# Kernel tuning notes

Measured on AMD Instinct MI355X. Metric: run time of the kernel, lower is better.

The kernel has to match this reference:

```python
import jax, jax.numpy as jnp
import numpy as np

N, C, H, W = 16, 256, 128, 128
TC = max(8, C // 32)  # temp_c
EPS = 1e-5


def setup_inputs() -> dict:
    key = jax.random.key(0)
    ks = jax.random.split(key, 10)
    x = jax.random.normal(ks[0], (N, C, H, W), jnp.float32)
    # conv1: 1x1, C -> TC (weight squeezed to [TC, C])
    w1 = jax.random.normal(ks[1], (TC, C), jnp.float32) * 0.05
    b1 = jnp.zeros((TC,), jnp.float32)
    # BatchNorm2d (inference form)
    bn_gamma = jnp.ones((TC,), jnp.float32)
    bn_beta = jnp.zeros((TC,), jnp.float32)
    bn_mean = jnp.zeros((TC,), jnp.float32)
    bn_var = jnp.ones((TC,), jnp.float32)
    # conv2: kernel (1,2), TC -> C, squeezed to [C, TC, 2]
    w2 = jax.random.normal(ks[2], (C, TC, 2), jnp.float32) * 0.1
    b2 = jnp.zeros((C,), jnp.float32)
    # conv3: kernel (2,1), TC -> C, squeezed to [C, TC, 2]
    w3 = jax.random.normal(ks[3], (C, TC, 2), jnp.float32) * 0.1
    b3 = jnp.zeros((C,), jnp.float32)
    # conv4: kernel (1,2), TC -> C, squeezed to [C, TC, 2]
    w4 = jax.random.normal(ks[4], (C, TC, 2), jnp.float32) * 0.1
    b4 = jnp.zeros((C,), jnp.float32)
    return dict(x=x, w1=w1, b1=b1, bn_gamma=bn_gamma, bn_beta=bn_beta,
                bn_mean=bn_mean, bn_var=bn_var, w2=w2, b2=b2, w3=w3, b3=b3,
                w4=w4, b4=b4)


def reference(x, w1, b1, bn_gamma, bn_beta, bn_mean, bn_var,
              w2, b2, w3, b3, w4, b4):
    n, c, Hh, Ww = x.shape
    # avg/max pools along W (per-row), H (per-col), and global (per-channel)
    cat_h = jnp.stack([x.mean(3), x.max(3)], axis=-1)            # [n,c,H,2]
    cat_w = jnp.stack([x.mean(2), x.max(2)], axis=-1)            # [n,c,W,2]
    cat_c = jnp.stack([x.mean((2, 3)), x.max((2, 3))], -1)[:, :, None, :]  # [n,c,1,2]
    x_cat = jnp.concatenate([cat_h, cat_w, cat_c], axis=2)       # [n,c,H+W+1,2]
    # 1x1 conv + BN (inference) + h_swish
    y = jnp.einsum('ncsk,tc->ntsk', x_cat, w1) + b1[None, :, None, None]
    inv = bn_gamma / jnp.sqrt(bn_var + EPS)
    y = (y - bn_mean[None, :, None, None]) * inv[None, :, None, None] \
        + bn_beta[None, :, None, None]
    y = y * jnp.clip(y + 3.0, 0.0, 6.0) / 6.0                    # h_swish
    # split
    xh = y[:, :, :Hh, :]               # [n,tc,H,2]
    xw = y[:, :, Hh:Hh + Ww, :]        # [n,tc,W,2]
    xc = y[:, :, Hh + Ww, :]           # [n,tc,2]
    # tiny convs (kernels collapse to contractions over (tc, k)) + sigmoid
    a_h = jax.nn.sigmoid(jnp.einsum('nthk,otk->noh', xh, w2) + b2[None, :, None])  # [n,C,H]
    a_w = jax.nn.sigmoid(jnp.einsum('ntwk,otk->now', xw, w3) + b3[None, :, None])  # [n,C,W]
    a_c = jax.nn.sigmoid(jnp.einsum('ntk,otk->no', xc, w4) + b4[None, :])          # [n,C]
    return x * a_w[:, :, None, :] * a_h[:, :, :, None] * a_c[:, :, None, None]
```

## Files before the change

### kernel.cpp

```cpp
#include <hip/hip_runtime.h>
#include <math.h>

#define N_ 16
#define C_ 256
#define H_ 128
#define W_ 128
#define TC_ 8
#define S_ 257
#define EPS_ 1e-5f
#define NBLK 512
#define BPN 32

#define XCT_OFF  0
#define AH_OFF   2105344
#define AW_OFF   (AH_OFF + 524288)
#define Y256_OFF (AW_OFF + 524288)

typedef float f4n __attribute__((ext_vector_type(4)));

template <int CTRL>
__device__ __forceinline__ float dpp_zf(float x) {
    return __int_as_float(__builtin_amdgcn_update_dpp(
        0, __float_as_int(x), CTRL, 0xF, 0xF, true));
}
template <int CTRL>
__device__ __forceinline__ float dpp_keep(float x) {
    return __int_as_float(__builtin_amdgcn_update_dpp(
        __float_as_int(x), __float_as_int(x), CTRL, 0xF, 0xF, false));
}
#define SHR1 0x111
#define SHR2 0x112
#define SHR4 0x114
#define SHR8 0x118
#define BC15 0x142

__device__ __forceinline__ float rowsum32(float x) {
    x += dpp_zf<SHR1>(x);
    x += dpp_zf<SHR2>(x);
    x += dpp_zf<SHR4>(x);
    x += dpp_zf<SHR8>(x);
    x += dpp_zf<BC15>(x);
    return x;
}
__device__ __forceinline__ float rowmax32(float x) {
    x = fmaxf(x, dpp_keep<SHR1>(x));
    x = fmaxf(x, dpp_keep<SHR2>(x));
    x = fmaxf(x, dpp_keep<SHR4>(x));
    x = fmaxf(x, dpp_keep<SHR8>(x));
    x = fmaxf(x, dpp_keep<BC15>(x));
    return x;
}

__global__ __launch_bounds__(256, 4) void k1_stats(
    const float* __restrict__ x, float* __restrict__ xcat)
{
    const int tid = threadIdx.x, lane = tid & 63, wv = tid >> 6;
    const int p = blockIdx.x * 4 + wv;
    const float4* xt = reinterpret_cast<const float4*>(x) + (size_t)p * 4096;
    float2* xcat2 = reinterpret_cast<float2*>(xcat) + (size_t)p * S_;

    float4 cs = make_float4(0.f, 0.f, 0.f, 0.f);
    float4 cm = make_float4(-INFINITY, -INFINITY, -INFINITY, -INFINITY);

    #pragma unroll 8
    for (int it = 0; it < 64; ++it) {
        const float4 v = xt[it * 64 + lane];
        cs.x += v.x; cs.y += v.y; cs.z += v.z; cs.w += v.w;
        cm.x = fmaxf(cm.x, v.x); cm.y = fmaxf(cm.y, v.y);
        cm.z = fmaxf(cm.z, v.z); cm.w = fmaxf(cm.w, v.w);

        float rs = (v.x + v.y) + (v.z + v.w);
        float rm = fmaxf(fmaxf(v.x, v.y), fmaxf(v.z, v.w));
        rs = rowsum32(rs);
        rm = rowmax32(rm);
        if ((lane & 31) == 31)
            xcat2[it * 2 + (lane >> 5)] = make_float2(rs * (1.f / 128.f), rm);
    }

    cs.x += __shfl_xor(cs.x, 32); cs.y += __shfl_xor(cs.y, 32);
    cs.z += __shfl_xor(cs.z, 32); cs.w += __shfl_xor(cs.w, 32);
    cm.x = fmaxf(cm.x, __shfl_xor(cm.x, 32));
    cm.y = fmaxf(cm.y, __shfl_xor(cm.y, 32));
    cm.z = fmaxf(cm.z, __shfl_xor(cm.z, 32));
    cm.w = fmaxf(cm.w, __shfl_xor(cm.w, 32));

    if (lane < 32) {
        const int w0 = 4 * lane;
        xcat2[128 + w0 + 0] = make_float2(cs.x * (1.f / 128.f), cm.x);
        xcat2[128 + w0 + 1] = make_float2(cs.y * (1.f / 128.f), cm.y);
        xcat2[128 + w0 + 2] = make_float2(cs.z * (1.f / 128.f), cm.z);
        xcat2[128 + w0 + 3] = make_float2(cs.w * (1.f / 128.f), cm.w);
    }

    float gs = (cs.x + cs.y) + (cs.z + cs.w);
    float gm = fmaxf(fmaxf(cm.x, cm.y), fmaxf(cm.z, cm.w));
    #pragma unroll
    for (int m = 16; m >= 1; m >>= 1) {
        gs += __shfl_xor(gs, m);
        gm = fmaxf(gm, __shfl_xor(gm, m));
    }
    if (lane == 0) xcat2[256] = make_float2(gs * (1.f / 16384.f), gm);
}

__global__ __launch_bounds__(256, 2) void k2_attn(
    const float* __restrict__ xcat,
    const float* __restrict__ w1, const float* __restrict__ b1,
    const float* __restrict__ gam, const float* __restrict__ bet,
    const float* __restrict__ mu, const float* __restrict__ var,
    const float* __restrict__ w2, const float* __restrict__ b2,
    const float* __restrict__ w3, const float* __restrict__ b3,
    float* __restrict__ ahg, float* __restrict__ awg, float* __restrict__ y256g)
{
    const int b = blockIdx.x;
    const int n = b >> 5, cg = b & 31;
    const int tid = threadIdx.x;
    __shared__ __align__(16) float smf[6448];

    float* w1s = smf;
    float* red = smf + 2048;
    float* ys  = smf + 6272;
    const float2* xc2 = reinterpret_cast<const float2*>(xcat) + (size_t)n * C_ * S_;
    const int s0 = cg * 8;

    for (int i = tid; i < TC_ * C_; i += 256) w1s[i] = w1[i];
    __syncthreads();

    {
        const int cgrp = tid >> 3, si = tid & 7;
        const int s = s0 + si;
        float acc[16];
        #pragma unroll
        for (int j = 0; j < 16; ++j) acc[j] = 0.f;
        #pragma unroll
        for (int i = 0; i < 8; ++i) {
            const int c = cgrp * 8 + i;
            const float2 v = xc2[c * S_ + s];
            #pragma unroll
            for (int t = 0; t < TC_; ++t) {
                const float w = w1s[t * C_ + c];
                acc[t * 2 + 0] += v.x * w;
                acc[t * 2 + 1] += v.y * w;
            }
        }
        #pragma unroll
        for (int j = 0; j < 16; ++j) red[(si * 16 + j) * 33 + cgrp] = acc[j];
    }
    __syncthreads();

    if (tid < 128) {
        const int si2 = tid >> 4, j = tid & 15, t = j >> 1;
        float z = 0.f;
        #pragma unroll
        for (int g = 0; g < 32; ++g) z += red[(si2 * 16 + j) * 33 + g];
        const float inv = gam[t] * rsqrtf(var[t] + EPS_);
        float y = (z + b1[t] - mu[t]) * inv + bet[t];
        y = y * fminf(fmaxf(y + 3.f, 0.f), 6.f) * (1.f / 6.f);
        ys[si2 * 17 + j] = y;
    }
    __syncthreads();

    if (cg == BPN - 1) {
        const int c = tid;
        const float2 v = xc2[c * S_ + 256];
        float pj[16];
        #pragma unroll
        for (int t = 0; t < TC_; ++t) {
            const float w = w1s[t * C_ + c];
            pj[t * 2 + 0] = v.x * w;
            pj[t * 2 + 1] = v.y * w;
        }
        __syncthreads();
        float* red2 = smf;
        float* redB = smf + 4400;
        #pragma unroll
        for (int j = 0; j < 16; ++j) red2[tid * 17 + j] = pj[j];
        __syncthreads();
        {
            const int g = tid >> 4, j = tid & 15;
            float z = 0.f;
            #pragma unroll
            for (int m = 0; m < 16; ++m) z += red2[(g * 16 + m) * 17 + j];
            redB[j * 17 + g] = z;
        }
        __syncthreads();
        if (tid < 16) {
            const int j = tid, t = j >> 1;
            float z = 0.f;
            #pragma unroll
            for (int g = 0; g < 16; ++g) z += redB[j * 17 + g];
            const float inv = gam[t] * rsqrtf(var[t] + EPS_);
            float y = (z + b1[t] - mu[t]) * inv + bet[t];
            y = y * fminf(fmaxf(y + 3.f, 0.f), 6.f) * (1.f / 6.f);
            y256g[n * 16 + j] = y;
        }
        __syncthreads();
    }

    {
        const int o = tid;
        const bool is_h = (cg < 16);
        const float* wX = is_h ? w2 : w3;
        const float zb = is_h ? b2[o] : b3[o];
        float4 wr[4];
        const float4* wv = reinterpret_cast<const float4*>(wX + o * 16);
        #pragma unroll
        for (int q = 0; q < 4; ++q) wr[q] = wv[q];

        float r[8];
        #pragma unroll
        for (int si = 0; si < 8; ++si) {
            float z = zb;
            #pragma unroll
            for (int q = 0; q < 4; ++q) {
                z += ys[si * 17 + q * 4 + 0] * wr[q].x
                   + ys[si * 17 + q * 4 + 1] * wr[q].y
                   + ys[si * 17 + q * 4 + 2] * wr[q].z
                   + ys[si * 17 + q * 4 + 3] * wr[q].w;
            }
            r[si] = 1.f / (1.f + expf(-z));
        }
        float* og = is_h ? (ahg + (size_t)(n * C_ + o) * H_ + s0)
                         : (awg + (size_t)(n * C_ + o) * W_ + (s0 - 128));
        *reinterpret_cast<float4*>(og)     = make_float4(r[0], r[1], r[2], r[3]);
        *reinterpret_cast<float4*>(og + 4) = make_float4(r[4], r[5], r[6], r[7]);
    }
}

__global__ __launch_bounds__(256, 4) void k3_apply(
    const float* __restrict__ x,
    const float* __restrict__ w4, const float* __restrict__ b4,
    const float* __restrict__ ahg, const float* __restrict__ awg,
    const float* __restrict__ y256g, float* __restrict__ out)
{
    const int tid = threadIdx.x, lane = tid & 63, wv = tid >> 6;
    const int p = blockIdx.x * 4 + wv;
    const int n = p >> 8, o = p & 255;

    float z = b4[o];
    const float4* w4v = reinterpret_cast<const float4*>(w4 + o * 16);
    const float4* yv  = reinterpret_cast<const float4*>(y256g + n * 16);
    #pragma unroll
    for (int q = 0; q < 4; ++q) {
        const float4 ww = w4v[q], yy = yv[q];
        z += yy.x * ww.x + yy.y * ww.y + yy.z * ww.z + yy.w * ww.w;
    }
    const float ac = 1.f / (1.f + expf(-z));

    const float4 aw = reinterpret_cast<const float4*>(awg + (size_t)p * W_)[lane & 31];

    const f4n* x4 = reinterpret_cast<const f4n*>(x) + (size_t)p * 4096;
    f4n* o4 = reinterpret_cast<f4n*>(out) + (size_t)p * 4096;
    const float* ah = ahg + (size_t)p * H_;
    const int half = lane >> 5;

    #pragma unroll 8
    for (int it = 0; it < 64; ++it) {
        f4n v = x4[it * 64 + lane];
        const float s = ac * ah[2 * it + half];
        v.x *= s * aw.x; v.y *= s * aw.y; v.z *= s * aw.z; v.w *= s * aw.w;
        __builtin_nontemporal_store(v, &o4[it * 64 + lane]);
    }
}

extern "C" void kernel_launch(void* const* d_in, const int* in_sizes, int n_in,
                              void* d_out, int out_size, void* d_ws, size_t ws_size,
                              hipStream_t stream) {
    const float* x   = (const float*)d_in[0];
    const float* w1  = (const float*)d_in[1];
    const float* b1  = (const float*)d_in[2];
    const float* gam = (const float*)d_in[3];
    const float* bet = (const float*)d_in[4];
    const float* mu  = (const float*)d_in[5];
    const float* var = (const float*)d_in[6];
    const float* w2  = (const float*)d_in[7];
    const float* b2  = (const float*)d_in[8];
    const float* w3  = (const float*)d_in[9];
    const float* b3  = (const float*)d_in[10];
    const float* w4  = (const float*)d_in[11];
    const float* b4  = (const float*)d_in[12];

    float* ws    = (float*)d_ws;
    float* xcat  = ws + XCT_OFF;
    float* ahg   = ws + AH_OFF;
    float* awg   = ws + AW_OFF;
    float* y256g = ws + Y256_OFF;
    float* out   = (float*)d_out;

    k1_stats<<<1024, 256, 0, stream>>>(x, xcat);
    k2_attn<<<NBLK, 256, 0, stream>>>(xcat, w1, b1, gam, bet, mu, var,
                                      w2, b2, w3, b3, ahg, awg, y256g);
    k3_apply<<<1024, 256, 0, stream>>>(x, w4, b4, ahg, awg, y256g, out);
}
```

Before: 155.2 us.

## Fuse three kernels into one persistent kernel with per-batch atomic barriers

The three launches (stats, attention, apply) become one kernel with one block per (n,c) plane. Each block holds its 64KB plane in registers, so x is read from HBM only once instead of twice. Per-batch global atomic counters act as barriers between the stats, attention and apply phases, and a memset resets them each call. The kernel needs all 4096 blocks to be co-resident or it can deadlock, and the register-held tile plus spin waits may reduce occupancy.

```diff
diff --git a/kernel.cpp b/kernel.cpp
--- a/kernel.cpp
+++ b/kernel.cpp
@@ -8,13 +8,13 @@
 #define TC_ 8
 #define S_ 257
 #define EPS_ 1e-5f
-#define NBLK 512
-#define BPN 32
+#define NBLK 4096
 
 #define XCT_OFF  0
 #define AH_OFF   2105344
 #define AW_OFF   (AH_OFF + 524288)
 #define Y256_OFF (AW_OFF + 524288)
+#define CNT_OFF  (Y256_OFF + 256)
 
 typedef float f4n __attribute__((ext_vector_type(4)));
 
@@ -51,20 +51,34 @@
     return x;
 }
 
-__global__ __launch_bounds__(256, 4) void k1_stats(
-    const float* __restrict__ x, float* __restrict__ xcat)
+__global__ __launch_bounds__(256, 4) void mega(
+    const float* __restrict__ x,
+    const float* __restrict__ w1, const float* __restrict__ b1,
+    const float* __restrict__ gam, const float* __restrict__ bet,
+    const float* __restrict__ mu, const float* __restrict__ var,
+    const float* __restrict__ w2, const float* __restrict__ b2,
+    const float* __restrict__ w3, const float* __restrict__ b3,
+    const float* __restrict__ w4, const float* __restrict__ b4,
+    float* __restrict__ xcat, float* __restrict__ ahg, float* __restrict__ awg,
+    float* __restrict__ y256g, unsigned* __restrict__ cnt,
+    float* __restrict__ out)
 {
+    const int b = blockIdx.x;
+    const int n = b >> 8, c = b & 255;
     const int tid = threadIdx.x, lane = tid & 63, wv = tid >> 6;
-    const int p = blockIdx.x * 4 + wv;
-    const float4* xt = reinterpret_cast<const float4*>(x) + (size_t)p * 4096;
-    float2* xcat2 = reinterpret_cast<float2*>(xcat) + (size_t)p * S_;
-
+    __shared__ __align__(16) float smf[6448];
+
+    const f4n* x4 = reinterpret_cast<const f4n*>(x) + (size_t)b * 4096;
+    float2* xcat2 = reinterpret_cast<float2*>(xcat) + (size_t)b * S_;
+
+    f4n xr[16];
     float4 cs = make_float4(0.f, 0.f, 0.f, 0.f);
     float4 cm = make_float4(-INFINITY, -INFINITY, -INFINITY, -INFINITY);
 
-    #pragma unroll 8
-    for (int it = 0; it < 64; ++it) {
-        const float4 v = xt[it * 64 + lane];
+    #pragma unroll
+    for (int it = 0; it < 16; ++it) {
+        xr[it] = x4[it * 256 + tid];
+        const f4n v = xr[it];
         cs.x += v.x; cs.y += v.y; cs.z += v.z; cs.w += v.w;
         cm.x = fmaxf(cm.x, v.x); cm.y = fmaxf(cm.y, v.y);
         cm.z = fmaxf(cm.z, v.z); cm.w = fmaxf(cm.w, v.w);
@@ -74,7 +88,8 @@
         rs = rowsum32(rs);
         rm = rowmax32(rm);
         if ((lane & 31) == 31)
-            xcat2[it * 2 + (lane >> 5)] = make_float2(rs * (1.f / 128.f), rm);
+            xcat2[it * 8 + wv * 2 + (lane >> 5)] =
+                make_float2(rs * (1.f / 128.f), rm);
     }
 
     cs.x += __shfl_xor(cs.x, 32); cs.y += __shfl_xor(cs.y, 32);
@@ -84,181 +99,203 @@
     cm.z = fmaxf(cm.z, __shfl_xor(cm.z, 32));
     cm.w = fmaxf(cm.w, __shfl_xor(cm.w, 32));
 
-    if (lane < 32) {
-        const int w0 = 4 * lane;
-        xcat2[128 + w0 + 0] = make_float2(cs.x * (1.f / 128.f), cm.x);
-        xcat2[128 + w0 + 1] = make_float2(cs.y * (1.f / 128.f), cm.y);
-        xcat2[128 + w0 + 2] = make_float2(cs.z * (1.f / 128.f), cm.z);
-        xcat2[128 + w0 + 3] = make_float2(cs.w * (1.f / 128.f), cm.w);
-    }
-
-    float gs = (cs.x + cs.y) + (cs.z + cs.w);
-    float gm = fmaxf(fmaxf(cm.x, cm.y), fmaxf(cm.z, cm.w));
-    #pragma unroll
-    for (int m = 16; m >= 1; m >>= 1) {
-        gs += __shfl_xor(gs, m);
-        gm = fmaxf(gm, __shfl_xor(gm, m));
-    }
-    if (lane == 0) xcat2[256] = make_float2(gs * (1.f / 16384.f), gm);
-}
-
-__global__ __launch_bounds__(256, 2) void k2_attn(
-    const float* __restrict__ xcat,
-    const float* __restrict__ w1, const float* __restrict__ b1,
-    const float* __restrict__ gam, const float* __restrict__ bet,
-    const float* __restrict__ mu, const float* __restrict__ var,
-    const float* __restrict__ w2, const float* __restrict__ b2,
-    const float* __restrict__ w3, const float* __restrict__ b3,
-    float* __restrict__ ahg, float* __restrict__ awg, float* __restrict__ y256g)
-{
-    const int b = blockIdx.x;
-    const int n = b >> 5, cg = b & 31;
-    const int tid = threadIdx.x;
-    __shared__ __align__(16) float smf[6448];
-
-    float* w1s = smf;
-    float* red = smf + 2048;
-    float* ys  = smf + 6272;
-    const float2* xc2 = reinterpret_cast<const float2*>(xcat) + (size_t)n * C_ * S_;
-    const int s0 = cg * 8;
-
-    for (int i = tid; i < TC_ * C_; i += 256) w1s[i] = w1[i];
+    {
+        float4* scr_s = reinterpret_cast<float4*>(smf);
+        float4* scr_m = reinterpret_cast<float4*>(smf) + 128;
+        if (lane < 32) {
+            scr_s[wv * 32 + lane] = make_float4(cs.x, cs.y, cs.z, cs.w);
+            scr_m[wv * 32 + lane] = make_float4(cm.x, cm.y, cm.z, cm.w);
+        }
+        __syncthreads();
+
+        if (tid < 32) {
+            const float4 s0 = scr_s[tid],      s1 = scr_s[32 + tid],
+                         s2 = scr_s[64 + tid], s3 = scr_s[96 + tid];
+            const float4 m0 = scr_m[tid],      m1 = scr_m[32 + tid],
+                         m2 = scr_m[64 + tid], m3 = scr_m[96 + tid];
+            float4 S, M;
+            S.x = (s0.x + s1.x) + (s2.x + s3.x);
+            S.y = (s0.y + s1.y) + (s2.y + s3.y);
+            S.z = (s0.z + s1.z) + (s2.z + s3.z);
+            S.w = (s0.w + s1.w) + (s2.w + s3.w);
+            M.x = fmaxf(fmaxf(m0.x, m1.x), fmaxf(m2.x, m3.x));
+            M.y = fmaxf(fmaxf(m0.y, m1.y), fmaxf(m2.y, m3.y));
+            M.z = fmaxf(fmaxf(m0.z, m1.z), fmaxf(m2.z, m3.z));
+            M.w = fmaxf(fmaxf(m0.w, m1.w), fmaxf(m2.w, m3.w));
+
+            const int w0 = 4 * tid;
+            xcat2[128 + w0 + 0] = make_float2(S.x * (1.f / 128.f), M.x);
+            xcat2[128 + w0 + 1] = make_float2(S.y * (1.f / 128.f), M.y);
+            xcat2[128 + w0 + 2] = make_float2(S.z * (1.f / 128.f), M.z);
+            xcat2[128 + w0 + 3] = make_float2(S.w * (1.f / 128.f), M.w);
+
+            float gs = (S.x + S.y) + (S.z + S.w);
+            float gm = fmaxf(fmaxf(M.x, M.y), fmaxf(M.z, M.w));
+            #pragma unroll
+            for (int m = 16; m >= 1; m >>= 1) {
+                gs += __shfl_xor(gs, m);
+                gm = fmaxf(gm, __shfl_xor(gm, m));
+            }
+            if (tid == 0) xcat2[256] = make_float2(gs * (1.f / 16384.f), gm);
+        }
+        __syncthreads();
+    }
+
+    if (tid == 0) {
+        unsigned* c1 = cnt + n * 64;
+        __hip_atomic_fetch_add(c1, 1u, __ATOMIC_RELEASE, __HIP_MEMORY_SCOPE_AGENT);
+        while (__hip_atomic_load(c1, __ATOMIC_RELAXED, __HIP_MEMORY_SCOPE_AGENT) < 256u)
+            __builtin_amdgcn_s_sleep(16);
+        (void)__hip_atomic_load(c1, __ATOMIC_ACQUIRE, __HIP_MEMORY_SCOPE_AGENT);
+    }
     __syncthreads();
 
-    {
-        const int cgrp = tid >> 3, si = tid & 7;
-        const int s = s0 + si;
-        float acc[16];
-        #pragma unroll
-        for (int j = 0; j < 16; ++j) acc[j] = 0.f;
-        #pragma unroll
-        for (int i = 0; i < 8; ++i) {
-            const int c = cgrp * 8 + i;
-            const float2 v = xc2[c * S_ + s];
-            #pragma unroll
-            for (int t = 0; t < TC_; ++t) {
-                const float w = w1s[t * C_ + c];
-                acc[t * 2 + 0] += v.x * w;
-                acc[t * 2 + 1] += v.y * w;
-            }
-        }
-        #pragma unroll
-        for (int j = 0; j < 16; ++j) red[(si * 16 + j) * 33 + cgrp] = acc[j];
-    }
-    __syncthreads();
-
-    if (tid < 128) {
-        const int si2 = tid >> 4, j = tid & 15, t = j >> 1;
-        float z = 0.f;
-        #pragma unroll
-        for (int g = 0; g < 32; ++g) z += red[(si2 * 16 + j) * 33 + g];
-        const float inv = gam[t] * rsqrtf(var[t] + EPS_);
-        float y = (z + b1[t] - mu[t]) * inv + bet[t];
-        y = y * fminf(fmaxf(y + 3.f, 0.f), 6.f) * (1.f / 6.f);
-        ys[si2 * 17 + j] = y;
-    }
-    __syncthreads();
-
-    if (cg == BPN - 1) {
-        const int c = tid;
-        const float2 v = xc2[c * S_ + 256];
-        float pj[16];
-        #pragma unroll
-        for (int t = 0; t < TC_; ++t) {
-            const float w = w1s[t * C_ + c];
-            pj[t * 2 + 0] = v.x * w;
-            pj[t * 2 + 1] = v.y * w;
-        }
-        __syncthreads();
-        float* red2 = smf;
-        float* redB = smf + 4400;
-        #pragma unroll
-        for (int j = 0; j < 16; ++j) red2[tid * 17 + j] = pj[j];
-        __syncthreads();
+    if (c < 32) {
+        float* w1s = smf;
+        float* red = smf + 2048;
+        float* ys  = smf + 6272;
+        const float2* xc2 = reinterpret_cast<const float2*>(xcat) + (size_t)n * C_ * S_;
+        const int s0 = c * 8;
+
+        for (int i = tid; i < TC_ * C_; i += 256) w1s[i] = w1[i];
+        __syncthreads();
+
         {
-            const int g = tid >> 4, j = tid & 15;
+            const int cgrp = tid >> 3, si = tid & 7;
+            const int s = s0 + si;
+            float acc[16];
+            #pragma unroll
+            for (int j = 0; j < 16; ++j) acc[j] = 0.f;
+            #pragma unroll
+            for (int i = 0; i < 8; ++i) {
+                const int cc = cgrp * 8 + i;
+                const float2 v = xc2[cc * S_ + s];
+                #pragma unroll
+                for (int t = 0; t < TC_; ++t) {
+                    const float w = w1s[t * C_ + cc];
+                    acc[t * 2 + 0] += v.x * w;
+                    acc[t * 2 + 1] += v.y * w;
+                }
+            }
+            #pragma unroll
+            for (int j = 0; j < 16; ++j) red[(si * 16 + j) * 33 + cgrp] = acc[j];
+        }
+        __syncthreads();
+
+        if (tid < 128) {
+            const int si2 = tid >> 4, j = tid & 15, t = j >> 1;
             float z = 0.f;
             #pragma unroll
-            for (int m = 0; m < 16; ++m) z += red2[(g * 16 + m) * 17 + j];
-            redB[j * 17 + g] = z;
-        }
-        __syncthreads();
-        if (tid < 16) {
-            const int j = tid, t = j >> 1;
-            float z = 0.f;
-            #pragma unroll
-            for (int g = 0; g < 16; ++g) z += redB[j * 17 + g];
+            for (int g = 0; g < 32; ++g) z += red[(si2 * 16 + j) * 33 + g];
             const float inv = gam[t] * rsqrtf(var[t] + EPS_);
             float y = (z + b1[t] - mu[t]) * inv + bet[t];
             y = y * fminf(fmaxf(y + 3.f, 0.f), 6.f) * (1.f / 6.f);
-            y256g[n * 16 + j] = y;
-        }
-        __syncthreads();
-    }
+            ys[si2 * 17 + j] = y;
+        }
+        __syncthreads();
+
+        if (c == 31) {
+            const int cc = tid;
+            const float2 v = xc2[cc * S_ + 256];
+            float pj[16];
+            #pragma unroll
+            for (int t = 0; t < TC_; ++t) {
+                const float w = w1s[t * C_ + cc];
+                pj[t * 2 + 0] = v.x * w;
+                pj[t * 2 + 1] = v.y * w;
+            }
+            __syncthreads();
+            float* red2 = smf;
+            float* redB = smf + 4400;
+            #pragma unroll
+            for (int j = 0; j < 16; ++j) red2[tid * 17 + j] = pj[j];
+            __syncthreads();
+            {
+                const int g = tid >> 4, j = tid & 15;
+                float z = 0.f;
+                #pragma unroll
+                for (int m = 0; m < 16; ++m) z += red2[(g * 16 + m) * 17 + j];
+                redB[j * 17 + g] = z;
+            }
+            __syncthreads();
+            if (tid < 16) {
+                const int j = tid, t = j >> 1;
+                float z = 0.f;
+                #pragma unroll
+                for (int g = 0; g < 16; ++g) z += redB[j * 17 + g];
+                const float inv = gam[t] * rsqrtf(var[t] + EPS_);
+                float y = (z + b1[t] - mu[t]) * inv + bet[t];
+                y = y * fminf(fmaxf(y + 3.f, 0.f), 6.f) * (1.f / 6.f);
+                y256g[n * 16 + j] = y;
+            }
+            __syncthreads();
+        }
+
+        {
+            const int o = tid;
+            const bool is_h = (c < 16);
+            const float* wX = is_h ? w2 : w3;
+            const float zb = is_h ? b2[o] : b3[o];
+            float4 wr[4];
+            const float4* wvp = reinterpret_cast<const float4*>(wX + o * 16);
+            #pragma unroll
+            for (int q = 0; q < 4; ++q) wr[q] = wvp[q];
+
+            float r[8];
+            #pragma unroll
+            for (int si = 0; si < 8; ++si) {
+                float z = zb;
+                #pragma unroll
+                for (int q = 0; q < 4; ++q) {
+                    z += ys[si * 17 + q * 4 + 0] * wr[q].x
+                       + ys[si * 17 + q * 4 + 1] * wr[q].y
+                       + ys[si * 17 + q * 4 + 2] * wr[q].z
+                       + ys[si * 17 + q * 4 + 3] * wr[q].w;
+                }
+                r[si] = 1.f / (1.f + expf(-z));
+            }
+            float* og = is_h ? (ahg + (size_t)(n * C_ + o) * H_ + s0)
+                             : (awg + (size_t)(n * C_ + o) * W_ + (s0 - 128));
+            *reinterpret_cast<float4*>(og)     = make_float4(r[0], r[1], r[2], r[3]);
+            *reinterpret_cast<float4*>(og + 4) = make_float4(r[4], r[5], r[6], r[7]);
+        }
+        __syncthreads();
+        if (tid == 0)
+            __hip_atomic_fetch_add(cnt + n * 64 + 32, 1u,
+                                   __ATOMIC_RELEASE, __HIP_MEMORY_SCOPE_AGENT);
+    }
+
+    if (tid == 0) {
+        unsigned* c2 = cnt + n * 64 + 32;
+        while (__hip_atomic_load(c2, __ATOMIC_RELAXED, __HIP_MEMORY_SCOPE_AGENT) < 32u)
+            __builtin_amdgcn_s_sleep(16);
+        (void)__hip_atomic_load(c2, __ATOMIC_ACQUIRE, __HIP_MEMORY_SCOPE_AGENT);
+    }
+    __syncthreads();
 
     {
-        const int o = tid;
-        const bool is_h = (cg < 16);
-        const float* wX = is_h ? w2 : w3;
-        const float zb = is_h ? b2[o] : b3[o];
-        float4 wr[4];
-        const float4* wv = reinterpret_cast<const float4*>(wX + o * 16);
+        float z = b4[c];
+        const float4* w4v = reinterpret_cast<const float4*>(w4 + c * 16);
+        const float4* yv  = reinterpret_cast<const float4*>(y256g + n * 16);
         #pragma unroll
-        for (int q = 0; q < 4; ++q) wr[q] = wv[q];
-
-        float r[8];
+        for (int q = 0; q < 4; ++q) {
+            const float4 ww = w4v[q], yy = yv[q];
+            z += yy.x * ww.x + yy.y * ww.y + yy.z * ww.z + yy.w * ww.w;
+        }
+        const float ac = 1.f / (1.f + expf(-z));
+
+        const float4 aw =
+            reinterpret_cast<const float4*>(awg + (size_t)b * W_)[tid & 31];
+        const float* ah = ahg + (size_t)b * H_;
+        f4n* o4 = reinterpret_cast<f4n*>(out) + (size_t)b * 4096;
+
         #pragma unroll
-        for (int si = 0; si < 8; ++si) {
-            float z = zb;
-            #pragma unroll
-            for (int q = 0; q < 4; ++q) {
-                z += ys[si * 17 + q * 4 + 0] * wr[q].x
-                   + ys[si * 17 + q * 4 + 1] * wr[q].y
-                   + ys[si * 17 + q * 4 + 2] * wr[q].z
-                   + ys[si * 17 + q * 4 + 3] * wr[q].w;
-            }
-            r[si] = 1.f / (1.f + expf(-z));
-        }
-        float* og = is_h ? (ahg + (size_t)(n * C_ + o) * H_ + s0)
-                         : (awg + (size_t)(n * C_ + o) * W_ + (s0 - 128));
-        *reinterpret_cast<float4*>(og)     = make_float4(r[0], r[1], r[2], r[3]);
-        *reinterpret_cast<float4*>(og + 4) = make_float4(r[4], r[5], r[6], r[7]);
-    }
-}
-
-__global__ __launch_bounds__(256, 4) void k3_apply(
-    const float* __restrict__ x,
-    const float* __restrict__ w4, const float* __restrict__ b4,
-    const float* __restrict__ ahg, const float* __restrict__ awg,
-    const float* __restrict__ y256g, float* __restrict__ out)
-{
-    const int tid = threadIdx.x, lane = tid & 63, wv = tid >> 6;
-    const int p = blockIdx.x * 4 + wv;
-    const int n = p >> 8, o = p & 255;
-
-    float z = b4[o];
-    const float4* w4v = reinterpret_cast<const float4*>(w4 + o * 16);
-    const float4* yv  = reinterpret_cast<const float4*>(y256g + n * 16);
-    #pragma unroll
-    for (int q = 0; q < 4; ++q) {
-        const float4 ww = w4v[q], yy = yv[q];
-        z += yy.x * ww.x + yy.y * ww.y + yy.z * ww.z + yy.w * ww.w;
-    }
-    const float ac = 1.f / (1.f + expf(-z));
-
-    const float4 aw = reinterpret_cast<const float4*>(awg + (size_t)p * W_)[lane & 31];
-
-    const f4n* x4 = reinterpret_cast<const f4n*>(x) + (size_t)p * 4096;
-    f4n* o4 = reinterpret_cast<f4n*>(out) + (size_t)p * 4096;
-    const float* ah = ahg + (size_t)p * H_;
-    const int half = lane >> 5;
-
-    #pragma unroll 8
-    for (int it = 0; it < 64; ++it) {
-        f4n v = x4[it * 64 + lane];
-        const float s = ac * ah[2 * it + half];
-        v.x *= s * aw.x; v.y *= s * aw.y; v.z *= s * aw.z; v.w *= s * aw.w;
-        __builtin_nontemporal_store(v, &o4[it * 64 + lane]);
+        for (int it = 0; it < 16; ++it) {
+            const float s = ac * ah[it * 8 + (tid >> 5)];
+            f4n v = xr[it];
+            v.x *= s * aw.x; v.y *= s * aw.y; v.z *= s * aw.z; v.w *= s * aw.w;
+            __builtin_nontemporal_store(v, &o4[it * 256 + tid]);
+        }
     }
 }
 
@@ -284,10 +321,11 @@
     float* ahg   = ws + AH_OFF;
     float* awg   = ws + AW_OFF;
     float* y256g = ws + Y256_OFF;
+    unsigned* cnt = (unsigned*)(ws + CNT_OFF);
     float* out   = (float*)d_out;
 
-    k1_stats<<<1024, 256, 0, stream>>>(x, xcat);
-    k2_attn<<<NBLK, 256, 0, stream>>>(xcat, w1, b1, gam, bet, mu, var,
-                                      w2, b2, w3, b3, ahg, awg, y256g);
-    k3_apply<<<1024, 256, 0, stream>>>(x, w4, b4, ahg, awg, y256g, out);
-}
+    hipMemsetAsync((void*)cnt, 0, 16 * 64 * sizeof(unsigned), stream);
+    mega<<<NBLK, 256, 0, stream>>>(x, w1, b1, gam, bet, mu, var,
+                                   w2, b2, w3, b3, w4, b4,
+                                   xcat, ahg, awg, y256g, cnt, out);
+}
```

Result: slower. 471.8 us (+204.0%).
